# Optimization experiments

Measured on AMD Instinct MI355X. Metric: run time of the kernel, lower is better.

The kernel has to match this reference:

```python
import jax, jax.numpy as jnp
import numpy as np

DIM = 1024
HEADS = 16
HEAD_DIM = DIM // HEADS
FFN = 4 * DIM
EPS = 1e-5


def layer_norm(x, g, b):
    mu = jnp.mean(x, axis=-1, keepdims=True)
    var = jnp.mean(jnp.square(x - mu), axis=-1, keepdims=True)
    return (x - mu) * jax.lax.rsqrt(var + EPS) * g + b


def setup_inputs() -> dict:
    key = jax.random.key(0)
    ks = jax.random.split(key, 12)
    s_d = 1.0 / np.sqrt(DIM)
    s_f = 1.0 / np.sqrt(FFN)
    return {
        "x": jax.random.normal(ks[0], (2, 2048, DIM), dtype=jnp.float32),
        "ln1_g": jnp.ones((DIM,), jnp.float32),
        "ln1_b": jnp.zeros((DIM,), jnp.float32),
        "q_w": jax.random.normal(ks[1], (DIM, DIM), jnp.float32) * s_d,
        "k_w": jax.random.normal(ks[2], (DIM, DIM), jnp.float32) * s_d,
        "v_w": jax.random.normal(ks[3], (DIM, DIM), jnp.float32) * s_d,
        "o_w": jax.random.normal(ks[4], (DIM, DIM), jnp.float32) * s_d,
        "ln2_g": jnp.ones((DIM,), jnp.float32),
        "ln2_b": jnp.zeros((DIM,), jnp.float32),
        "ffn_in_w": jax.random.normal(ks[5], (FFN, DIM), jnp.float32) * s_d,
        "ffn_in_b": jnp.zeros((FFN,), jnp.float32),
        "sw_w": jax.random.normal(ks[6], (FFN, FFN), jnp.float32) * s_f,
        "sw_v": jax.random.normal(ks[7], (FFN, FFN), jnp.float32) * s_f,
        "ffn_out_w": jax.random.normal(ks[8], (DIM, FFN), jnp.float32) * s_f,
        "ffn_out_b": jnp.zeros((DIM,), jnp.float32),
    }


def reference(x, ln1_g, ln1_b, q_w, k_w, v_w, o_w, ln2_g, ln2_b,
              ffn_in_w, ffn_in_b, sw_w, sw_v, ffn_out_w, ffn_out_b):
    B, L, D = x.shape
    scale = HEAD_DIM ** -0.5

    # --- attention block ---
    h = layer_norm(x, ln1_g, ln1_b)
    q = (h @ q_w.T).reshape(B, L, HEADS, HEAD_DIM).transpose(0, 2, 1, 3)
    k = (h @ k_w.T).reshape(B, L, HEADS, HEAD_DIM).transpose(0, 2, 1, 3)
    v = (h @ v_w.T).reshape(B, L, HEADS, HEAD_DIM).transpose(0, 2, 1, 3)
    attn = jnp.einsum("bhqd,bhkd->bhqk", q, k) * scale
    attn = jax.nn.softmax(attn, axis=-1)
    out = jnp.einsum("bhqk,bhkd->bhqd", attn, v)
    out = out.transpose(0, 2, 1, 3).reshape(B, L, D)
    x = x + out @ o_w.T

    # --- FFN block: Linear -> SwiGLU -> Linear ---
    h = layer_norm(x, ln2_g, ln2_b)
    u = h @ ffn_in_w.T + ffn_in_b                 # [B,L,FFN]
    g = jax.nn.silu(u @ sw_w.T) * (u @ sw_v.T)    # SwiGLU
    x = x + g @ ffn_out_w.T + ffn_out_b
    return x
```

## Files before the change

kernel.cpp:

```cpp
#include <hip/hip_runtime.h>
#include <hip/hip_bf16.h>

#define TOK 4096
#define DIM 1024
#define FFN_N 4096
#define SEQ 2048
#define HD 64

using short8 = __attribute__((ext_vector_type(8))) short;
using short4v = __attribute__((ext_vector_type(4))) short;
using f32x4 = __attribute__((ext_vector_type(4))) float;

__device__ __forceinline__ short f2b(float f){
  return __builtin_bit_cast(short, __float2bfloat16(f));
}
__device__ __forceinline__ float b2f(short s){
  return __bfloat162float(__builtin_bit_cast(__hip_bfloat16, s));
}

__device__ __forceinline__ void gl_lds16(const short* g, short* l){
  __builtin_amdgcn_global_load_lds(
      (const __attribute__((address_space(1))) unsigned int*)g,
      (__attribute__((address_space(3))) unsigned int*)l, 16, 0, 0);
}

#define BARRAW() asm volatile("s_barrier" ::: "memory")
#define VMCNT(n) asm volatile("s_waitcnt vmcnt(" #n ")" ::: "memory")

__global__ __launch_bounds__(256) void castk(const float* __restrict__ src,
                                             short* __restrict__ dst, int n){
  int stride = gridDim.x*256*4;
  for (int i = (blockIdx.x*256 + threadIdx.x)*4; i < n; i += stride){
    float4 v = *reinterpret_cast<const float4*>(src + i);
    short4v o; o[0]=f2b(v.x); o[1]=f2b(v.y); o[2]=f2b(v.z); o[3]=f2b(v.w);
    *reinterpret_cast<short4v*>(dst + i) = o;
  }
}

__global__ __launch_bounds__(256) void lnk(const float* __restrict__ x,
                                           const float* __restrict__ g,
                                           const float* __restrict__ b,
                                           short* __restrict__ out){
  int row = blockIdx.x;
  int t = threadIdx.x;
  const float* xr = x + (size_t)row*DIM;
  float4 v = *reinterpret_cast<const float4*>(xr + t*4);
  float s = v.x+v.y+v.z+v.w;
  float s2 = v.x*v.x+v.y*v.y+v.z*v.z+v.w*v.w;
  #pragma unroll
  for (int off=1; off<64; off<<=1){ s += __shfl_xor(s,off); s2 += __shfl_xor(s2,off); }
  __shared__ float as_[4], as2_[4];
  if ((t&63)==0){ as_[t>>6]=s; as2_[t>>6]=s2; }
  __syncthreads();
  s = as_[0]+as_[1]+as_[2]+as_[3];
  s2 = as2_[0]+as2_[1]+as2_[2]+as2_[3];
  float mu = s * (1.0f/DIM);
  float var = s2 * (1.0f/DIM) - mu*mu;
  float r = rsqrtf(var + 1e-5f);
  float4 gv = *reinterpret_cast<const float4*>(g + t*4);
  float4 bv = *reinterpret_cast<const float4*>(b + t*4);
  short4v o;
  o[0]=f2b((v.x-mu)*r*gv.x + bv.x);
  o[1]=f2b((v.y-mu)*r*gv.y + bv.y);
  o[2]=f2b((v.z-mu)*r*gv.z + bv.z);
  o[3]=f2b((v.w-mu)*r*gv.w + bv.w);
  *reinterpret_cast<short4v*>(out + (size_t)row*DIM + t*4) = o;
}

template<int MODE>
__global__ __launch_bounds__(256,2) void gemm_bt(
    const short* __restrict__ A, const short* __restrict__ Bt,
    short* __restrict__ Cb, float* __restrict__ Cf,
    const float* __restrict__ bias, const float* __restrict__ resid,
    const short* __restrict__ aux,
    int M, int N, int K)
{
  __shared__ __align__(16) short Al[128*32];
  __shared__ __align__(16) short Bl[128*32];
  const int tid = threadIdx.x, lane = tid & 63, w = tid >> 6;
  const int wr = w >> 1, wc = w & 1;
  const int bx = blockIdx.x, by = blockIdx.y;

  const short* ga0 = A  + (size_t)(by*128 + w*32 + (lane>>2))*K + (lane&3)*8;
  const short* gb0 = Bt + (size_t)(bx*128 + w*32 + (lane>>2))*K + (lane&3)*8;
  short* la0 = &Al[w*32*32];
  short* lb0 = &Bl[w*32*32];

  f32x4 acc[4][4] = {};

  for (int k0 = 0; k0 < K; k0 += 32){
    __syncthreads();
    gl_lds16(ga0 + k0,                 la0);
    gl_lds16(ga0 + k0 + (size_t)16*K,  la0 + 16*32);
    gl_lds16(gb0 + k0,                 lb0);
    gl_lds16(gb0 + k0 + (size_t)16*K,  lb0 + 16*32);
    __syncthreads();
    short8 af[4], bf[4];
    #pragma unroll
    for (int m=0;m<4;m++)
      af[m] = *reinterpret_cast<const short8*>(&Al[(wr*64 + m*16 + (lane&15))*32 + (lane>>4)*8]);
    #pragma unroll
    for (int n=0;n<4;n++)
      bf[n] = *reinterpret_cast<const short8*>(&Bl[(wc*64 + n*16 + (lane&15))*32 + (lane>>4)*8]);
    #pragma unroll
    for (int m=0;m<4;m++)
      #pragma unroll
      for (int n=0;n<4;n++)
        acc[m][n] = __builtin_amdgcn_mfma_f32_16x16x32_bf16(af[m], bf[n], acc[m][n], 0,0,0);
  }

  #pragma unroll
  for (int m=0;m<4;m++){
    #pragma unroll
    for (int n=0;n<4;n++){
      #pragma unroll
      for (int j=0;j<4;j++){
        int r = by*128 + wr*64 + m*16 + ((lane>>4)<<2) + j;
        int c = bx*128 + wc*64 + n*16 + (lane&15);
        float v = acc[m][n][j];
        if (MODE==1 || MODE==3) v += bias[c];
        size_t idx = (size_t)r*N + c;
        if (MODE==4){
          float a = b2f(aux[idx]);
          float sg = a / (1.0f + __expf(-a));
          Cb[idx] = f2b(sg * v);
        } else if (MODE<=1) {
          Cb[idx] = f2b(v);
        } else {
          Cf[idx] = resid[idx] + v;
        }
      }
    }
  }
}

template<int MODE>
__global__ __launch_bounds__(512,2) void gemm256(
    const short* __restrict__ A, const short* __restrict__ Bt,
    short* __restrict__ Cb,
    const float* __restrict__ bias, const short* __restrict__ aux,
    int M, int N, int K)
{
  __shared__ __align__(16) short L[65536];
  const int tid = threadIdx.x, lane = tid&63, w = tid>>6;
  const int q15 = lane&15, h8 = lane>>4;
  const int wm = w>>2, wn = w&3;
  const int NT = K>>6;

  int bid = blockIdx.x;
  int wg = (bid&7)*(gridDim.x>>3) + (bid>>3);
  const int by = wg >> 4, bx = wg & 15;

  const int isub = w*8 + (lane>>3);
  const int koff = ((lane&7) ^ ((lane>>3)&7))*8;

  const short* gA[2][2]; const short* gB[2][2];
  #pragma unroll
  for (int hh=0; hh<2; hh++){
    #pragma unroll
    for (int j=0; j<2; j++){
      int i = j*64 + isub;
      int Ra = by*256 + (i>>6)*128 + hh*64 + (i&63);
      gA[hh][j] = A + (size_t)Ra*K + koff;
      int Rb = bx*256 + (i>>5)*64 + hh*32 + (i&31);
      gB[hh][j] = Bt + (size_t)Rb*K + koff;
    }
  }

  auto stA = [&](int db, int hh, int j, int kt){
    gl_lds16(gA[hh][j] + (size_t)kt*64, &L[db*32768 + hh*8192 + j*4096 + w*512]);
  };
  auto stB = [&](int db, int hh, int j, int kt){
    gl_lds16(gB[hh][j] + (size_t)kt*64, &L[db*32768 + (2+hh)*8192 + j*4096 + w*512]);
  };
  auto rdA = [&](int db, int mh, int m, int ks)->short8{
    int i = wm*64 + m*16 + q15;
    int ch = (ks*4 + h8) ^ (i&7);
    return *reinterpret_cast<const short8*>(&L[db*32768 + mh*8192 + i*64 + ch*8]);
  };
  auto rdB = [&](int db, int nh, int n, int ks)->short8{
    int i = wn*32 + n*16 + q15;
    int ch = (ks*4 + h8) ^ (i&7);
    return *reinterpret_cast<const short8*>(&L[db*32768 + (2+nh)*8192 + i*64 + ch*8]);
  };

  f32x4 acc[8][4] = {};
  short8 af[4][2], bf[2][2];

#define MFMA_QUAD(MH, NH)                                                      \
  __builtin_amdgcn_s_setprio(1);                                               \
  _Pragma("unroll")                                                            \
  for (int m=0;m<4;m++){                                                       \
    _Pragma("unroll")                                                          \
    for (int n=0;n<2;n++){                                                     \
      acc[(MH)*4+m][(NH)*2+n] = __builtin_amdgcn_mfma_f32_16x16x32_bf16(       \
          af[m][0], bf[n][0], acc[(MH)*4+m][(NH)*2+n], 0,0,0);                 \
      acc[(MH)*4+m][(NH)*2+n] = __builtin_amdgcn_mfma_f32_16x16x32_bf16(       \
          af[m][1], bf[n][1], acc[(MH)*4+m][(NH)*2+n], 0,0,0);                 \
    }                                                                          \
  }                                                                            \
  __builtin_amdgcn_s_setprio(0);

  stA(0,0,0,0); stA(0,0,1,0);
  stB(0,0,0,0); stB(0,0,1,0);
  stA(0,1,0,0); stA(0,1,1,0);
  stB(0,1,0,0); stB(0,1,1,0);
  VMCNT(4);
  BARRAW();

  for (int t = 0; t < NT; ++t){
    const int db = t&1;
    const bool pf = (t+1 < NT);

    #pragma unroll
    for (int m=0;m<4;m++){ af[m][0]=rdA(db,0,m,0); af[m][1]=rdA(db,0,m,1); }
    #pragma unroll
    for (int n=0;n<2;n++){ bf[n][0]=rdB(db,0,n,0); bf[n][1]=rdB(db,0,n,1); }
    if (pf){ stA(db^1,0,0,t+1); stA(db^1,0,1,t+1); }
    BARRAW();
    MFMA_QUAD(0,0);
    if (pf){ VMCNT(2); } else { VMCNT(0); }
    BARRAW();

    #pragma unroll
    for (int n=0;n<2;n++){ bf[n][0]=rdB(db,1,n,0); bf[n][1]=rdB(db,1,n,1); }
    if (pf){ stB(db^1,0,0,t+1); stB(db^1,0,1,t+1); }
    BARRAW();
    MFMA_QUAD(0,1);
    BARRAW();

    #pragma unroll
    for (int m=0;m<4;m++){ af[m][0]=rdA(db,1,m,0); af[m][1]=rdA(db,1,m,1); }
    if (pf){ stA(db^1,1,0,t+1); stA(db^1,1,1,t+1); }
    BARRAW();
    MFMA_QUAD(1,1);
    BARRAW();

    #pragma unroll
    for (int n=0;n<2;n++){ bf[n][0]=rdB(db,0,n,0); bf[n][1]=rdB(db,0,n,1); }
    if (pf){ stB(db^1,1,0,t+1); stB(db^1,1,1,t+1); }
    BARRAW();
    MFMA_QUAD(1,0);
    if (pf){ VMCNT(4); }
    BARRAW();
  }

  #pragma unroll
  for (int mq=0;mq<8;mq++){
    #pragma unroll
    for (int nq=0;nq<4;nq++){
      #pragma unroll
      for (int jj=0;jj<4;jj++){
        int r = by*256 + wm*128 + mq*16 + h8*4 + jj;
        int c = bx*256 + wn*64  + nq*16 + q15;
        float v = acc[mq][nq][jj];
        if (MODE==1) v += bias[c];
        size_t idx = (size_t)r*N + c;
        if (MODE==4){
          float a = b2f(aux[idx]);
          float sg = a / (1.0f + __expf(-a));
          Cb[idx] = f2b(sg * v);
        } else {
          Cb[idx] = f2b(v);
        }
      }
    }
  }
#undef MFMA_QUAD
}

__global__ __launch_bounds__(256) void attnk(
    const short* __restrict__ Q, const short* __restrict__ K,
    const short* __restrict__ V, short* __restrict__ O)
{
  __shared__ __align__(16) short Kl[64*64];
  __shared__ __align__(16) short Vt[64*72];
  __shared__ __align__(16) short Pl[4*16*72];

  const int tid = threadIdx.x, lane = tid&63, w = tid>>6;
  const int h = lane>>4, q15 = lane&15;
  const int bh = blockIdx.y;
  const int b = bh >> 4, hd = bh & 15;
  const int q0 = blockIdx.x * 64;
  const size_t base = (size_t)b*SEQ*DIM + (size_t)hd*HD;

  short8 aq[2];
  {
    int qrow = q0 + w*16 + q15;
    const short* qp = Q + base + (size_t)qrow*DIM + h*8;
    aq[0] = *reinterpret_cast<const short8*>(qp);
    aq[1] = *reinterpret_cast<const short8*>(qp + 32);
  }

  float mrun[4], lrun[4];
  f32x4 o[4] = {};
  #pragma unroll
  for (int j=0;j<4;j++){ mrun[j] = -1e30f; lrun[j] = 0.f; }

  const int ksub = lane>>3;
  const int kchunk = (lane&7) ^ ksub;
  const short* kg0 = K + base + (size_t)(w*16 + ksub)*DIM + kchunk*8;
  const short* kg1 = kg0 + (size_t)8*DIM;
  short* kl_dst0 = &Kl[(w*16)*64];
  short* kl_dst1 = &Kl[(w*16 + 8)*64];

  const int vrow = tid>>2;
  const int vkc  = tid&3;
  const short* vg = V + base + (size_t)vrow*DIM + vkc*8;
  const int vmask = vkc<<4;

  short* plw = &Pl[w*16*72];
  const int pmaskw = h<<4;
  const int pmaskr = (q15>>2)<<4;

  for (int kv0 = 0; kv0 < SEQ; kv0 += 64){
    __syncthreads();
    gl_lds16(kg0 + (size_t)kv0*DIM, kl_dst0);
    gl_lds16(kg1 + (size_t)kv0*DIM, kl_dst1);
    short8 v0 = *reinterpret_cast<const short8*>(vg + (size_t)kv0*DIM);
    short8 v1 = *reinterpret_cast<const short8*>(vg + (size_t)kv0*DIM + 32);
    #pragma unroll
    for (int j=0;j<8;j++){
      int d0 = vkc*8 + j;
      Vt[d0*72 + (vrow ^ vmask)] = v0[j];
      Vt[(d0+32)*72 + (vrow ^ vmask)] = v1[j];
    }
    __syncthreads();

    f32x4 s[4];
    #pragma unroll
    for (int nt=0; nt<4; nt++){
      const short8 k0 = *reinterpret_cast<const short8*>(
          &Kl[(nt*16+q15)*64 + ((h       ^ (q15&7))*8)]);
      const short8 k1 = *reinterpret_cast<const short8*>(
          &Kl[(nt*16+q15)*64 + (((4+h)   ^ (q15&7))*8)]);
      f32x4 t = {};
      t = __builtin_amdgcn_mfma_f32_16x16x32_bf16(aq[0], k0, t, 0,0,0);
      t = __builtin_amdgcn_mfma_f32_16x16x32_bf16(aq[1], k1, t, 0,0,0);
      s[nt] = t * 0.125f;
    }

    float pm[4];
    #pragma unroll
    for (int j=0;j<4;j++)
      pm[j] = fmaxf(fmaxf(s[0][j],s[1][j]), fmaxf(s[2][j],s[3][j]));
    #pragma unroll
    for (int off=8; off>=1; off>>=1)
      #pragma unroll
      for (int j=0;j<4;j++) pm[j] = fmaxf(pm[j], __shfl_xor(pm[j], off));

    float al[4], rs[4];
    #pragma unroll
    for (int j=0;j<4;j++){
      float mn = fmaxf(mrun[j], pm[j]);
      al[j] = __expf(mrun[j]-mn);
      mrun[j] = mn;
      s[0][j] = __expf(s[0][j]-mn);
      s[1][j] = __expf(s[1][j]-mn);
      s[2][j] = __expf(s[2][j]-mn);
      s[3][j] = __expf(s[3][j]-mn);
      rs[j] = (s[0][j]+s[1][j]) + (s[2][j]+s[3][j]);
    }
    #pragma unroll
    for (int off=8; off>=1; off>>=1)
      #pragma unroll
      for (int j=0;j<4;j++) rs[j] += __shfl_xor(rs[j], off);
    #pragma unroll
    for (int j=0;j<4;j++) lrun[j] = lrun[j]*al[j] + rs[j];
    #pragma unroll
    for (int dt=0;dt<4;dt++)
      #pragma unroll
      for (int j=0;j<4;j++) o[dt][j] *= al[j];

    #pragma unroll
    for (int nt=0;nt<4;nt++)
      #pragma unroll
      for (int j=0;j<4;j++){
        int pr = 4*h + j;
        plw[pr*72 + ((nt*16 + q15) ^ pmaskw)] = f2b(s[nt][j]);
      }
    asm volatile("s_waitcnt lgkmcnt(0)" ::: "memory");
    const short8 ap0 = *reinterpret_cast<const short8*>(
        &plw[q15*72 + ((     h*8) ^ pmaskr)]);
    const short8 ap1 = *reinterpret_cast<const short8*>(
        &plw[q15*72 + ((32 + h*8) ^ pmaskr)]);
    #pragma unroll
    for (int dt=0;dt<4;dt++){
      int d = dt*16 + q15;
      int dm = ((d>>3)&3)<<4;
      const short8 vf0 = *reinterpret_cast<const short8*>(
          &Vt[d*72 + ((     h*8) ^ dm)]);
      const short8 vf1 = *reinterpret_cast<const short8*>(
          &Vt[d*72 + ((32 + h*8) ^ dm)]);
      o[dt] = __builtin_amdgcn_mfma_f32_16x16x32_bf16(ap0, vf0, o[dt], 0,0,0);
      o[dt] = __builtin_amdgcn_mfma_f32_16x16x32_bf16(ap1, vf1, o[dt], 0,0,0);
    }
  }

  #pragma unroll
  for (int dt=0;dt<4;dt++)
    #pragma unroll
    for (int j=0;j<4;j++){
      int qrow = q0 + w*16 + 4*h + j;
      O[base + (size_t)qrow*DIM + dt*16 + q15] = f2b(o[dt][j]/lrun[j]);
    }
}

extern "C" void kernel_launch(void* const* d_in, const int* in_sizes, int n_in,
                              void* d_out, int out_size, void* d_ws, size_t ws_size,
                              hipStream_t stream) {
  const float* x     = (const float*)d_in[0];
  const float* ln1_g = (const float*)d_in[1];
  const float* ln1_b = (const float*)d_in[2];
  const float* q_w   = (const float*)d_in[3];
  const float* k_w   = (const float*)d_in[4];
  const float* v_w   = (const float*)d_in[5];
  const float* o_w   = (const float*)d_in[6];
  const float* ln2_g = (const float*)d_in[7];
  const float* ln2_b = (const float*)d_in[8];
  const float* fi_w  = (const float*)d_in[9];
  const float* fi_b  = (const float*)d_in[10];
  const float* sw_w  = (const float*)d_in[11];
  const float* sw_v  = (const float*)d_in[12];
  const float* fo_w  = (const float*)d_in[13];
  const float* fo_b  = (const float*)d_in[14];
  float* out = (float*)d_out;

  char* W = (char*)d_ws;
  const size_t MB = 1024*1024;
  short* qw  = (short*)(W +   0*MB);
  short* kw  = (short*)(W +   2*MB);
  short* vw  = (short*)(W +   4*MB);
  short* ow  = (short*)(W +   6*MB);
  short* fiw = (short*)(W +   8*MB);
  short* sww = (short*)(W +  16*MB);
  short* swv = (short*)(W +  48*MB);
  short* fow = (short*)(W +  80*MB);
  short* hb  = (short*)(W +  88*MB);
  short* qb  = (short*)(W +  96*MB);
  short* kb  = (short*)(W + 104*MB);
  short* vb  = (short*)(W + 112*MB);
  short* ab  = (short*)(W + 120*MB);
  float* x2  = (float*)(W + 128*MB);
  short* ub  = (short*)(W + 144*MB);
  short* gb  = (short*)(W + 176*MB);
  short* a1  = (short*)(W +  96*MB);

  dim3 blk(256);
  castk<<<1024,blk,0,stream>>>(q_w, qw, 1024*1024);
  castk<<<1024,blk,0,stream>>>(k_w, kw, 1024*1024);
  castk<<<1024,blk,0,stream>>>(v_w, vw, 1024*1024);
  castk<<<1024,blk,0,stream>>>(o_w, ow, 1024*1024);
  castk<<<2048,blk,0,stream>>>(fi_w, fiw, 4096*1024);
  castk<<<2048,blk,0,stream>>>(sw_w, sww, 4096*4096);
  castk<<<2048,blk,0,stream>>>(sw_v, swv, 4096*4096);
  castk<<<2048,blk,0,stream>>>(fo_w, fow, 1024*4096);

  lnk<<<TOK,blk,0,stream>>>(x, ln1_g, ln1_b, hb);
  gemm_bt<0><<<dim3(8,32),blk,0,stream>>>(hb, qw, qb, nullptr, nullptr, nullptr, nullptr, TOK, DIM, DIM);
  gemm_bt<0><<<dim3(8,32),blk,0,stream>>>(hb, kw, kb, nullptr, nullptr, nullptr, nullptr, TOK, DIM, DIM);
  gemm_bt<0><<<dim3(8,32),blk,0,stream>>>(hb, vw, vb, nullptr, nullptr, nullptr, nullptr, TOK, DIM, DIM);
  attnk<<<dim3(32,32),blk,0,stream>>>(qb, kb, vb, ab);
  gemm_bt<2><<<dim3(8,32),blk,0,stream>>>(ab, ow, nullptr, x2, nullptr, x, nullptr, TOK, DIM, DIM);
  lnk<<<TOK,blk,0,stream>>>(x2, ln2_g, ln2_b, hb);
  gemm256<1><<<256, 512, 0, stream>>>(hb, fiw, ub, fi_b, nullptr, TOK, FFN_N, DIM);
  gemm256<0><<<256, 512, 0, stream>>>(ub, sww, a1, nullptr, nullptr, TOK, FFN_N, FFN_N);
  gemm256<4><<<256, 512, 0, stream>>>(ub, swv, gb, nullptr, a1, TOK, FFN_N, FFN_N);
  gemm_bt<3><<<dim3(8,32),blk,0,stream>>>(gb, fow, nullptr, out, fo_b, x2, nullptr, TOK, DIM, FFN_N);
}
```

Measured before the change: 675.4 us.

## Pre-transpose V globally and swap QK^T MFMA operands to simplify softmax

Adds a separate kernel that writes V transposed per head into workspace, so the attention kernel can load both K and V tiles with direct global-to-LDS copies instead of scalar scatter stores. The QK^T MFMA operands are swapped so each lane holds one query column, which reduces the softmax max and sum reductions to two cross-lane shuffles and uses packed bf16 conversion for P stores. This costs an extra kernel launch and an extra round trip of V through memory, and it relies on the transposed-layout indexing being correct.

```diff
diff --git a/kernel.cpp b/kernel.cpp
--- a/kernel.cpp
+++ b/kernel.cpp
@@ -16,6 +16,11 @@
 }
 __device__ __forceinline__ float b2f(short s){
   return __bfloat162float(__builtin_bit_cast(__hip_bfloat16, s));
+}
+__device__ __forceinline__ unsigned cvtpk(float lo, float hi){
+  unsigned r;
+  asm("v_cvt_pk_bf16_f32 %0, %1, %2" : "=v"(r) : "v"(lo), "v"(hi));
+  return r;
 }
 
 __device__ __forceinline__ void gl_lds16(const short* g, short* l){
@@ -269,12 +274,40 @@
 #undef MFMA_QUAD
 }
 
+__global__ __launch_bounds__(256) void vtrk(const short* __restrict__ V,
+                                            short* __restrict__ Vt){
+  __shared__ __align__(16) short T[64*72];
+  const int tid = threadIdx.x;
+  const int bh = blockIdx.y;
+  const int b = bh >> 4, hd = bh & 15;
+  const int t0 = blockIdx.x * 64;
+  const short* src = V + (size_t)b*SEQ*DIM + (size_t)hd*HD;
+
+  const int r = tid>>2, c = tid&3;
+  short8 a0 = *reinterpret_cast<const short8*>(src + (size_t)(t0+r)*DIM + c*8);
+  short8 a1 = *reinterpret_cast<const short8*>(src + (size_t)(t0+r)*DIM + (c+4)*8);
+  *reinterpret_cast<short8*>(&T[r*72 + c*8]) = a0;
+  *reinterpret_cast<short8*>(&T[r*72 + (c+4)*8]) = a1;
+  __syncthreads();
+
+  short* dst = Vt + (size_t)bh*HD*SEQ;
+  #pragma unroll
+  for (int dd=0; dd<2; dd++){
+    int d = (tid>>3) + dd*32;
+    int tc = tid&7;
+    short8 o;
+    #pragma unroll
+    for (int j=0;j<8;j++) o[j] = T[(tc*8+j)*72 + d];
+    *reinterpret_cast<short8*>(dst + (size_t)d*SEQ + t0 + tc*8) = o;
+  }
+}
+
 __global__ __launch_bounds__(256) void attnk(
     const short* __restrict__ Q, const short* __restrict__ K,
-    const short* __restrict__ V, short* __restrict__ O)
+    const short* __restrict__ Vt, short* __restrict__ O)
 {
   __shared__ __align__(16) short Kl[64*64];
-  __shared__ __align__(16) short Vt[64*72];
+  __shared__ __align__(16) short Vl[64*64];
   __shared__ __align__(16) short Pl[4*16*72];
 
   const int tid = threadIdx.x, lane = tid&63, w = tid>>6;
@@ -283,6 +316,7 @@
   const int b = bh >> 4, hd = bh & 15;
   const int q0 = blockIdx.x * 64;
   const size_t base = (size_t)b*SEQ*DIM + (size_t)hd*HD;
+  const size_t vbase = (size_t)bh*HD*SEQ;
 
   short8 aq[2];
   {
@@ -292,117 +326,106 @@
     aq[1] = *reinterpret_cast<const short8*>(qp + 32);
   }
 
-  float mrun[4], lrun[4];
+  float mrun = -1e30f, lrun = 0.f;
   f32x4 o[4] = {};
-  #pragma unroll
-  for (int j=0;j<4;j++){ mrun[j] = -1e30f; lrun[j] = 0.f; }
 
   const int ksub = lane>>3;
   const int kchunk = (lane&7) ^ ksub;
   const short* kg0 = K + base + (size_t)(w*16 + ksub)*DIM + kchunk*8;
   const short* kg1 = kg0 + (size_t)8*DIM;
-  short* kl_dst0 = &Kl[(w*16)*64];
-  short* kl_dst1 = &Kl[(w*16 + 8)*64];
-
-  const int vrow = tid>>2;
-  const int vkc  = tid&3;
-  const short* vg = V + base + (size_t)vrow*DIM + vkc*8;
-  const int vmask = vkc<<4;
+  const short* vg0 = Vt + vbase + (size_t)(w*16 + ksub)*SEQ + kchunk*8;
+  const short* vg1 = vg0 + (size_t)8*SEQ;
+  short* kl0 = &Kl[(w*16)*64];
+  short* kl1 = &Kl[(w*16 + 8)*64];
+  short* vl0 = &Vl[(w*16)*64];
+  short* vl1 = &Vl[(w*16 + 8)*64];
 
   short* plw = &Pl[w*16*72];
-  const int pmaskw = h<<4;
-  const int pmaskr = (q15>>2)<<4;
+  const int xk = (q15&7);
 
   for (int kv0 = 0; kv0 < SEQ; kv0 += 64){
     __syncthreads();
-    gl_lds16(kg0 + (size_t)kv0*DIM, kl_dst0);
-    gl_lds16(kg1 + (size_t)kv0*DIM, kl_dst1);
-    short8 v0 = *reinterpret_cast<const short8*>(vg + (size_t)kv0*DIM);
-    short8 v1 = *reinterpret_cast<const short8*>(vg + (size_t)kv0*DIM + 32);
-    #pragma unroll
-    for (int j=0;j<8;j++){
-      int d0 = vkc*8 + j;
-      Vt[d0*72 + (vrow ^ vmask)] = v0[j];
-      Vt[(d0+32)*72 + (vrow ^ vmask)] = v1[j];
-    }
+    gl_lds16(kg0 + (size_t)kv0*DIM, kl0);
+    gl_lds16(kg1 + (size_t)kv0*DIM, kl1);
+    gl_lds16(vg0 + kv0, vl0);
+    gl_lds16(vg1 + kv0, vl1);
     __syncthreads();
 
     f32x4 s[4];
     #pragma unroll
     for (int nt=0; nt<4; nt++){
-      const short8 k0 = *reinterpret_cast<const short8*>(
-          &Kl[(nt*16+q15)*64 + ((h       ^ (q15&7))*8)]);
-      const short8 k1 = *reinterpret_cast<const short8*>(
-          &Kl[(nt*16+q15)*64 + (((4+h)   ^ (q15&7))*8)]);
+      const short8 kf0 = *reinterpret_cast<const short8*>(
+          &Kl[(nt*16+q15)*64 + ((h    ^ xk)*8)]);
+      const short8 kf1 = *reinterpret_cast<const short8*>(
+          &Kl[(nt*16+q15)*64 + (((4+h)^ xk)*8)]);
       f32x4 t = {};
-      t = __builtin_amdgcn_mfma_f32_16x16x32_bf16(aq[0], k0, t, 0,0,0);
-      t = __builtin_amdgcn_mfma_f32_16x16x32_bf16(aq[1], k1, t, 0,0,0);
+      t = __builtin_amdgcn_mfma_f32_16x16x32_bf16(kf0, aq[0], t, 0,0,0);
+      t = __builtin_amdgcn_mfma_f32_16x16x32_bf16(kf1, aq[1], t, 0,0,0);
       s[nt] = t * 0.125f;
     }
 
-    float pm[4];
-    #pragma unroll
-    for (int j=0;j<4;j++)
-      pm[j] = fmaxf(fmaxf(s[0][j],s[1][j]), fmaxf(s[2][j],s[3][j]));
-    #pragma unroll
-    for (int off=8; off>=1; off>>=1)
-      #pragma unroll
-      for (int j=0;j<4;j++) pm[j] = fmaxf(pm[j], __shfl_xor(pm[j], off));
-
-    float al[4], rs[4];
-    #pragma unroll
-    for (int j=0;j<4;j++){
-      float mn = fmaxf(mrun[j], pm[j]);
-      al[j] = __expf(mrun[j]-mn);
-      mrun[j] = mn;
-      s[0][j] = __expf(s[0][j]-mn);
-      s[1][j] = __expf(s[1][j]-mn);
-      s[2][j] = __expf(s[2][j]-mn);
-      s[3][j] = __expf(s[3][j]-mn);
-      rs[j] = (s[0][j]+s[1][j]) + (s[2][j]+s[3][j]);
-    }
-    #pragma unroll
-    for (int off=8; off>=1; off>>=1)
-      #pragma unroll
-      for (int j=0;j<4;j++) rs[j] += __shfl_xor(rs[j], off);
-    #pragma unroll
-    for (int j=0;j<4;j++) lrun[j] = lrun[j]*al[j] + rs[j];
+    float pm = s[0][0];
+    #pragma unroll
+    for (int nt=0; nt<4; nt++)
+      #pragma unroll
+      for (int j=0; j<4; j++) pm = fmaxf(pm, s[nt][j]);
+    pm = fmaxf(pm, __shfl_xor(pm, 16));
+    pm = fmaxf(pm, __shfl_xor(pm, 32));
+
+    float mn = fmaxf(mrun, pm);
+    float al = __expf(mrun - mn);
+    mrun = mn;
+    float rs = 0.f;
+    #pragma unroll
+    for (int nt=0; nt<4; nt++)
+      #pragma unroll
+      for (int j=0; j<4; j++){
+        s[nt][j] = __expf(s[nt][j] - mn);
+        rs += s[nt][j];
+      }
+    rs += __shfl_xor(rs, 16);
+    rs += __shfl_xor(rs, 32);
+    lrun = lrun*al + rs;
+
+    float alj[4];
+    #pragma unroll
+    for (int j=0;j<4;j++) alj[j] = __shfl(al, 4*h + j);
     #pragma unroll
     for (int dt=0;dt<4;dt++)
       #pragma unroll
-      for (int j=0;j<4;j++) o[dt][j] *= al[j];
-
-    #pragma unroll
-    for (int nt=0;nt<4;nt++)
-      #pragma unroll
-      for (int j=0;j<4;j++){
-        int pr = 4*h + j;
-        plw[pr*72 + ((nt*16 + q15) ^ pmaskw)] = f2b(s[nt][j]);
-      }
+      for (int j=0;j<4;j++) o[dt][j] *= alj[j];
+
+    #pragma unroll
+    for (int nt=0;nt<4;nt++){
+      uint2 u;
+      u.x = cvtpk(s[nt][0], s[nt][1]);
+      u.y = cvtpk(s[nt][2], s[nt][3]);
+      *reinterpret_cast<uint2*>(&plw[q15*72 + nt*16 + 4*h]) = u;
+    }
     asm volatile("s_waitcnt lgkmcnt(0)" ::: "memory");
-    const short8 ap0 = *reinterpret_cast<const short8*>(
-        &plw[q15*72 + ((     h*8) ^ pmaskr)]);
-    const short8 ap1 = *reinterpret_cast<const short8*>(
-        &plw[q15*72 + ((32 + h*8) ^ pmaskr)]);
+    const short8 ap0 = *reinterpret_cast<const short8*>(&plw[q15*72 +      h*8]);
+    const short8 ap1 = *reinterpret_cast<const short8*>(&plw[q15*72 + 32 + h*8]);
+
     #pragma unroll
     for (int dt=0;dt<4;dt++){
-      int d = dt*16 + q15;
-      int dm = ((d>>3)&3)<<4;
       const short8 vf0 = *reinterpret_cast<const short8*>(
-          &Vt[d*72 + ((     h*8) ^ dm)]);
+          &Vl[(dt*16+q15)*64 + ((h    ^ xk)*8)]);
       const short8 vf1 = *reinterpret_cast<const short8*>(
-          &Vt[d*72 + ((32 + h*8) ^ dm)]);
+          &Vl[(dt*16+q15)*64 + (((4+h)^ xk)*8)]);
       o[dt] = __builtin_amdgcn_mfma_f32_16x16x32_bf16(ap0, vf0, o[dt], 0,0,0);
       o[dt] = __builtin_amdgcn_mfma_f32_16x16x32_bf16(ap1, vf1, o[dt], 0,0,0);
     }
   }
 
+  float rl[4];
+  #pragma unroll
+  for (int j=0;j<4;j++) rl[j] = 1.0f / __shfl(lrun, 4*h + j);
   #pragma unroll
   for (int dt=0;dt<4;dt++)
     #pragma unroll
     for (int j=0;j<4;j++){
       int qrow = q0 + w*16 + 4*h + j;
-      O[base + (size_t)qrow*DIM + dt*16 + q15] = f2b(o[dt][j]/lrun[j]);
+      O[base + (size_t)qrow*DIM + dt*16 + q15] = f2b(o[dt][j]*rl[j]);
     }
 }
 
@@ -445,6 +468,7 @@
   short* ub  = (short*)(W + 144*MB);
   short* gb  = (short*)(W + 176*MB);
   short* a1  = (short*)(W +  96*MB);
+  short* vt  = (short*)(W + 144*MB);
 
   dim3 blk(256);
   castk<<<1024,blk,0,stream>>>(q_w, qw, 1024*1024);
@@ -460,7 +484,8 @@
   gemm_bt<0><<<dim3(8,32),blk,0,stream>>>(hb, qw, qb, nullptr, nullptr, nullptr, nullptr, TOK, DIM, DIM);
   gemm_bt<0><<<dim3(8,32),blk,0,stream>>>(hb, kw, kb, nullptr, nullptr, nullptr, nullptr, TOK, DIM, DIM);
   gemm_bt<0><<<dim3(8,32),blk,0,stream>>>(hb, vw, vb, nullptr, nullptr, nullptr, nullptr, TOK, DIM, DIM);
-  attnk<<<dim3(32,32),blk,0,stream>>>(qb, kb, vb, ab);
+  vtrk<<<dim3(SEQ/64,32),blk,0,stream>>>(vb, vt);
+  attnk<<<dim3(32,32),blk,0,stream>>>(qb, kb, vt, ab);
   gemm_bt<2><<<dim3(8,32),blk,0,stream>>>(ab, ow, nullptr, x2, nullptr, x, nullptr, TOK, DIM, DIM);
   lnk<<<TOK,blk,0,stream>>>(x2, ln2_g, ln2_b, hb);
   gemm256<1><<<256, 512, 0, stream>>>(hb, fiw, ub, fi_b, nullptr, TOK, FFN_N, DIM);
```

Result: faster. 627.3 us (-7.1%).
